# Optimization experiments

Hardware: AMD Instinct MI355X
Metric: run time of the kernel (lower is better)

## Reference

```python
import jax, jax.numpy as jnp
import numpy as np

H = 128           # hidden_size
N_NODE = 100000   # item vocab
B = 1024          # sessions
NODES_PER = 50
N = B * NODES_PER # total session nodes
E = 8 * N         # edges


def setup_inputs() -> dict:
    key = jax.random.key(0)
    ks = jax.random.split(key, 16)
    stdv = 1.0 / np.sqrt(H)
    u = lambda k, shape: jax.random.uniform(k, shape, jnp.float32, -stdv, stdv)
    x = jax.random.randint(ks[0], (N,), 1, N_NODE + 1)      # 1-indexed items
    edge_index = jax.random.randint(ks[1], (2, E), 0, N)
    batch = jnp.repeat(jnp.arange(B), NODES_PER)            # sorted segment ids
    return {
        "x": x, "edge_index": edge_index, "batch": batch,
        "emb_weight": u(ks[2], (N_NODE, H)),
        "W_gconv": u(ks[3], (H, H)),
        "W_ih": u(ks[4], (3 * H, H)), "W_hh": u(ks[5], (3 * H, H)),
        "b_ih": u(ks[6], (3 * H,)), "b_hh": u(ks[7], (3 * H,)),
        "W1_w": u(ks[8], (H, H)), "W1_b": u(ks[9], (H,)),
        "W2_w": u(ks[10], (H, H)), "W2_b": u(ks[11], (H,)),
        "q_w": u(ks[12], (1, H)), "q_b": u(ks[13], (1,)),
        "W3_w": u(ks[14], (H, 2 * H)), "W3_b": u(ks[15], (H,)),
    }


def _forward(x, edge_index, batch, emb_weight, W_gconv, W_ih, W_hh, b_ih, b_hh,
             W1_w, W1_b, W2_w, W2_b, q_w, q_b, W3_w, W3_b):
    n = x.shape[0]
    h = emb_weight[x - 1]                                   # [N, H]
    # GatedGraphConv, num_layers=1: linear -> scatter-add -> GRUCell
    m = h @ W_gconv                                          # [N, H]
    agg = jax.ops.segment_sum(m[edge_index[0]], edge_index[1], num_segments=n)
    gi = agg @ W_ih.T + b_ih                                 # [N, 3H]
    gh = h @ W_hh.T + b_hh
    i_r, i_z, i_n = jnp.split(gi, 3, axis=1)
    h_r, h_z, h_n = jnp.split(gh, 3, axis=1)
    r = jax.nn.sigmoid(i_r + h_r)
    z = jax.nn.sigmoid(i_z + h_z)
    ng = jnp.tanh(i_n + r * h_n)
    h = (1.0 - z) * ng + z * h
    h = jax.nn.relu(h)
    # Embedding2Score: segment-wise attention readout
    last_idx = jax.ops.segment_max(jnp.arange(n), batch, num_segments=B)
    v_n = h[last_idx]                                        # [B, H] last node per session
    a = jax.nn.sigmoid(v_n[batch] @ W1_w.T + W1_b + h @ W2_w.T + W2_b)
    alpha = a @ q_w.T + q_b                                  # [N, 1]
    s_g = jax.ops.segment_sum(alpha * h, batch, num_segments=B)  # [B, H]
    s_h = jnp.concatenate([v_n, s_g], axis=1) @ W3_w.T + W3_b    # [B, H]
    return s_h @ emb_weight.T                                # [B, n_node]


def reference(x, edge_index, batch, emb_weight, W_gconv, W_ih, W_hh, b_ih, b_hh,
              W1_w, W1_b, W2_w, W2_b, q_w, q_b, W3_w, W3_b):
    return _forward(x, edge_index, batch, emb_weight, W_gconv, W_ih, W_hh, b_ih, b_hh,
                    W1_w, W1_b, W2_w, W2_b, q_w, q_b, W3_w, W3_b)
```

## Files before the change

### kernel.cpp

```cpp
#include <hip/hip_runtime.h>
#include <math.h>

#define NNODES 51200
#define NEDGES 409600
#define NB 1024
#define NODES_PER 50
#define NVOCAB 100000
#define NVPAD 100096
#define SLOTS 64

typedef __attribute__((ext_vector_type(8))) short bf16x8;
typedef __attribute__((ext_vector_type(4))) float f32x4;

__device__ __forceinline__ float sigf(float x) { return 1.0f / (1.0f + __expf(-x)); }

__device__ __forceinline__ ushort f2bf(float x) {
    union { float f; unsigned u; } v; v.f = x;
    const unsigned r = v.u + 0x7FFF + ((v.u >> 16) & 1);
    return (ushort)(r >> 16);
}
__device__ __forceinline__ float bf2f(ushort u) {
    union { float f; unsigned u; } v; v.u = ((unsigned)u) << 16; return v.f;
}
__device__ __forceinline__ bf16x8 cvt8(const float* __restrict__ src) {
    const float4 v0 = *(const float4*)src, v1 = *(const float4*)(src + 4);
    bf16x8 p;
    p[0] = (short)f2bf(v0.x); p[1] = (short)f2bf(v0.y);
    p[2] = (short)f2bf(v0.z); p[3] = (short)f2bf(v0.w);
    p[4] = (short)f2bf(v1.x); p[5] = (short)f2bf(v1.y);
    p[6] = (short)f2bf(v1.z); p[7] = (short)f2bf(v1.w);
    return p;
}

__global__ __launch_bounds__(256)
void prep_kernel(const int* __restrict__ x, const float* __restrict__ emb,
                 ushort* __restrict__ hb, const int* __restrict__ ei,
                 int* __restrict__ cnt, int* __restrict__ esrc,
                 ushort* __restrict__ embswz, const float* __restrict__ Wih,
                 const float* __restrict__ Wg, ushort* __restrict__ Wc) {
    const int bid = blockIdx.x;
    const int t = threadIdx.x;
    if (bid < 3200) {
        const int tid = bid * 256 + t;
        const int i = tid >> 4, c8 = (tid & 15) * 8;
        const int idx = x[i] - 1;
        *(bf16x8*)(hb + (size_t)i * 128 + c8) = cvt8(emb + (size_t)idx * 128 + c8);
    } else if (bid < 4800) {
        const int e = (bid - 3200) * 256 + t;
        const int dst = ei[NEDGES + e];
        const int pos = atomicAdd(&cnt[dst], 1);
        if (pos < SLOTS) esrc[(size_t)dst * SLOTS + pos] = ei[e];
    } else if (bid < 11056) {
        const int f = (bid - 4800) * 256 + t;
        const int row = f >> 4, c8 = (f & 15) * 8;
        bf16x8 pk = {0, 0, 0, 0, 0, 0, 0, 0};
        if (row < NVOCAB) pk = cvt8(emb + (size_t)row * 128 + c8);
        *(bf16x8*)&embswz[(size_t)row * 128 + (c8 ^ ((row & 7) << 3))] = pk;
    } else {
        const int idx = (bid - 11056) * 256 + t;
        const int mrow = idx >> 7, n = idx & 127;
        const float* wr = Wih + (size_t)mrow * 128;
        const float* gr = Wg + (size_t)n * 128;
        float acc = 0.f;
        #pragma unroll 8
        for (int k = 0; k < 128; ++k)
            acc = fmaf(wr[k], gr[k], acc);
        Wc[idx] = f2bf(acc);
    }
}

__global__ __launch_bounds__(256)
void agg_kernel(const int* __restrict__ cnt, const int* __restrict__ esrc,
                const ushort* __restrict__ hb, ushort* __restrict__ aggb) {
    const int node = blockIdx.x * 4 + (threadIdx.x >> 6);
    const int l = threadIdx.x & 63;
    int cn = cnt[node]; if (cn > SLOTS) cn = SLOTS;
    const int* es = esrc + (size_t)node * SLOTS;
    float ax = 0.f, ay = 0.f;
    for (int j = 0; j < cn; ++j) {
        const int src = es[j];
        const unsigned u = *(const unsigned*)(hb + (size_t)src * 128 + l * 2);
        ax += bf2f((ushort)(u & 0xffff));
        ay += bf2f((ushort)(u >> 16));
    }
    const unsigned o = (unsigned)f2bf(ax) | ((unsigned)f2bf(ay) << 16);
    *(unsigned*)(aggb + (size_t)node * 128 + l * 2) = o;
}

__global__ __launch_bounds__(512)
void gru_fused(const ushort* __restrict__ aggb, const ushort* __restrict__ Wc,
               const float* __restrict__ Whh, const float* __restrict__ bih,
               const float* __restrict__ bhh, ushort* __restrict__ hb) {
    __shared__ ushort As[128 * 128];
    __shared__ ushort Bs[384 * 128];
    const int m0 = blockIdx.x * 128;
    const int t = threadIdx.x;
    const int lane = t & 63, wid = t >> 6;
    const int l15 = lane & 15, kg = (lane >> 4) * 8;

    #pragma unroll
    for (int f = t; f < 2048; f += 512) {
        const int r = f >> 4, c8 = (f & 15) * 8;
        const bf16x8 pk = *(const bf16x8*)(aggb + (size_t)(m0 + r) * 128 + c8);
        *(bf16x8*)&As[r * 128 + (c8 ^ ((r & 7) << 3))] = pk;
    }
    #pragma unroll
    for (int f = t; f < 6144; f += 512) {
        const int r = f >> 4, c8 = (f & 15) * 8;
        const bf16x8 pk = *(const bf16x8*)(Wc + (size_t)r * 128 + c8);
        *(bf16x8*)&Bs[r * 128 + (c8 ^ ((r & 7) << 3))] = pk;
    }
    __syncthreads();

    f32x4 gi[24] = {};
    #pragma unroll
    for (int kc = 0; kc < 4; ++kc) {
        const int cs = kc * 32 + kg;
        const int ra = wid * 16 + l15;
        const bf16x8 af = *(const bf16x8*)&As[ra * 128 + (cs ^ ((ra & 7) << 3))];
        #pragma unroll
        for (int j = 0; j < 24; ++j) {
            const int rb = j * 16 + l15;
            const bf16x8 bfr = *(const bf16x8*)&Bs[rb * 128 + (cs ^ ((rb & 7) << 3))];
            gi[j] = __builtin_amdgcn_mfma_f32_16x16x32_bf16(af, bfr, gi[j], 0, 0, 0);
        }
    }
    __syncthreads();

    #pragma unroll
    for (int f = t; f < 2048; f += 512) {
        const int r = f >> 4, c8 = (f & 15) * 8;
        const bf16x8 pk = *(const bf16x8*)(hb + (size_t)(m0 + r) * 128 + c8);
        *(bf16x8*)&As[r * 128 + (c8 ^ ((r & 7) << 3))] = pk;
    }
    #pragma unroll
    for (int f = t; f < 6144; f += 512) {
        const int r = f >> 4, c8 = (f & 15) * 8;
        *(bf16x8*)&Bs[r * 128 + (c8 ^ ((r & 7) << 3))] = cvt8(Whh + (size_t)r * 128 + c8);
    }
    __syncthreads();

    f32x4 gh[24] = {};
    #pragma unroll
    for (int kc = 0; kc < 4; ++kc) {
        const int cs = kc * 32 + kg;
        const int ra = wid * 16 + l15;
        const bf16x8 af = *(const bf16x8*)&As[ra * 128 + (cs ^ ((ra & 7) << 3))];
        #pragma unroll
        for (int j = 0; j < 24; ++j) {
            const int rb = j * 16 + l15;
            const bf16x8 bfr = *(const bf16x8*)&Bs[rb * 128 + (cs ^ ((rb & 7) << 3))];
            gh[j] = __builtin_amdgcn_mfma_f32_16x16x32_bf16(af, bfr, gh[j], 0, 0, 0);
        }
    }

    const int lr0 = wid * 16 + (lane >> 4) * 4;
    #pragma unroll
    for (int j = 0; j < 8; ++j) {
        const int col = j * 16 + l15;
        const float bir = bih[col], biz = bih[128 + col], bin = bih[256 + col];
        const float bhr = bhh[col], bhz = bhh[128 + col], bhn = bhh[256 + col];
        #pragma unroll
        for (int q = 0; q < 4; ++q) {
            const int lr = lr0 + q;
            const int adr = lr * 128 + (col ^ ((lr & 7) << 3));
            const float hv = bf2f(As[adr]);
            const float r_ = sigf(gi[j][q] + bir + gh[j][q] + bhr);
            const float z  = sigf(gi[j + 8][q] + biz + gh[j + 8][q] + bhz);
            const float ng = tanhf(gi[j + 16][q] + bin + r_ * (gh[j + 16][q] + bhn));
            As[adr] = f2bf(fmaxf((1.f - z) * ng + z * hv, 0.f));
        }
    }
    __syncthreads();
    #pragma unroll
    for (int f = t; f < 2048; f += 512) {
        const int r = f >> 4, c8 = (f & 15) * 8;
        *(bf16x8*)(hb + (size_t)(m0 + r) * 128 + c8) =
            *(const bf16x8*)&As[r * 128 + (c8 ^ ((r & 7) << 3))];
    }
}

__global__ __launch_bounds__(256)
void attn_sh(const ushort* __restrict__ hb, const float* __restrict__ W1,
             const float* __restrict__ b1, const float* __restrict__ W2,
             const float* __restrict__ qw, const float* __restrict__ qbp,
             const float* __restrict__ b2, const float* __restrict__ W3,
             const float* __restrict__ b3, ushort* __restrict__ shb) {
    __shared__ ushort As[128 * 128];
    __shared__ ushort Bs[128 * 128];
    __shared__ float t1s[2][128];
    __shared__ float qws[128];
    __shared__ float apar[2][2][64];
    __shared__ float alph[2][64];
    __shared__ float sgs[2][128];
    const int m0 = blockIdx.x * 100;
    const int t = threadIdx.x;
    const int lane = t & 63, wid = t >> 6;
    const int wr = wid >> 1, wc = wid & 1;
    const int l15 = lane & 15, kg = (lane >> 4) * 8;
    const int cr0 = (lane >> 4) * 4;

    #pragma unroll
    for (int f = t; f < 2048; f += 256) {
        const int r = f >> 4, c8 = (f & 15) * 8;
        int gr = m0 + r; if (gr > NNODES - 1) gr = NNODES - 1;
        *(bf16x8*)&As[r * 128 + (c8 ^ ((r & 7) << 3))] =
            *(const bf16x8*)(hb + (size_t)gr * 128 + c8);
        *(bf16x8*)&Bs[r * 128 + (c8 ^ ((r & 7) << 3))] = cvt8(W2 + (size_t)r * 128 + c8);
    }
    if (t < 128) qws[t] = qw[t];
    __syncthreads();

    f32x4 acc[4][4] = {};
    #pragma unroll
    for (int kc = 0; kc < 4; ++kc) {
        const int cs = kc * 32 + kg;
        bf16x8 af[4], bfr[4];
        #pragma unroll
        for (int i = 0; i < 4; ++i) {
            const int ra = wr * 64 + i * 16 + l15;
            af[i] = *(const bf16x8*)&As[ra * 128 + (cs ^ ((ra & 7) << 3))];
            const int rb = wc * 64 + i * 16 + l15;
            bfr[i] = *(const bf16x8*)&Bs[rb * 128 + (cs ^ ((rb & 7) << 3))];
        }
        #pragma unroll
        for (int i = 0; i < 4; ++i)
            #pragma unroll
            for (int j = 0; j < 4; ++j)
                acc[i][j] = __builtin_amdgcn_mfma_f32_16x16x32_bf16(af[i], bfr[j], acc[i][j], 0, 0, 0);
    }
    __syncthreads();

    #pragma unroll
    for (int j = 0; j < 4; ++j) {
        const int col = wc * 64 + j * 16 + l15;
        const int csw = (col & 7) << 3;
        #pragma unroll
        for (int i = 0; i < 4; ++i) {
            const int row = wr * 64 + i * 16 + cr0;
            #pragma unroll
            for (int q = 0; q < 4; ++q)
                Bs[col * 128 + ((row + q) ^ csw)] = f2bf(acc[i][j][q]);
        }
    }

    const int sess = wid >> 1, half = wid & 1;
    const int d = half * 64 + lane;
    const int vrow = sess * 50 + 49;
    const int vsw = (vrow & 7) << 3;
    float t1v = b1[d] + b2[d];
    const float* w1r = W1 + (size_t)d * 128;
    #pragma unroll 8
    for (int k = 0; k < 128; k += 4) {
        const float4 w = *(const float4*)(w1r + k);
        t1v += w.x * bf2f(As[vrow * 128 + ((k + 0) ^ vsw)])
             + w.y * bf2f(As[vrow * 128 + ((k + 1) ^ vsw)])
             + w.z * bf2f(As[vrow * 128 + ((k + 2) ^ vsw)])
             + w.w * bf2f(As[vrow * 128 + ((k + 3) ^ vsw)]);
    }
    t1s[sess][d] = t1v;
    __syncthreads();

    float p = 0.f;
    if (lane < 50) {
        const int row = sess * 50 + lane;
        const int d0 = half * 64;
        #pragma unroll 8
        for (int dd = d0; dd < d0 + 64; ++dd)
            p += qws[dd] * sigf(t1s[sess][dd] + bf2f(Bs[dd * 128 + (row ^ ((dd & 7) << 3))]));
    }
    apar[sess][half][lane] = p;
    __syncthreads();
    if (half == 0 && lane < 50)
        alph[sess][lane] = apar[sess][0][lane] + apar[sess][1][lane] + qbp[0];
    __syncthreads();

    float sacc = 0.f;
    #pragma unroll 10
    for (int i = 0; i < 50; ++i) {
        const int row = sess * 50 + i;
        sacc += alph[sess][i] * bf2f(As[row * 128 + (d ^ ((row & 7) << 3))]);
    }
    sgs[sess][d] = sacc;
    __syncthreads();

    float shacc = b3[d];
    const float* w3r = W3 + (size_t)d * 256;
    #pragma unroll 8
    for (int k = 0; k < 128; k += 4) {
        const float4 w = *(const float4*)(w3r + k);
        shacc += w.x * bf2f(As[vrow * 128 + ((k + 0) ^ vsw)])
               + w.y * bf2f(As[vrow * 128 + ((k + 1) ^ vsw)])
               + w.z * bf2f(As[vrow * 128 + ((k + 2) ^ vsw)])
               + w.w * bf2f(As[vrow * 128 + ((k + 3) ^ vsw)]);
    }
    #pragma unroll 8
    for (int k = 0; k < 128; k += 4) {
        const float4 w = *(const float4*)(w3r + 128 + k);
        shacc += w.x * sgs[sess][k] + w.y * sgs[sess][k + 1]
               + w.z * sgs[sess][k + 2] + w.w * sgs[sess][k + 3];
    }
    const int orow = blockIdx.x * 2 + sess;
    shb[(size_t)orow * 128 + (d ^ ((orow & 7) << 3))] = f2bf(shacc);
}

__global__ __launch_bounds__(256)
void gemm_vocab(float* __restrict__ C, const ushort* __restrict__ Ab,
                const ushort* __restrict__ Bswz) {
    __shared__ ushort As[128 * 128];
    __shared__ ushort Bs[128 * 128];
    float* Cs = (float*)Bs;
    const int id = blockIdx.x;
    const int xcd = id & 7, loc = id >> 3;
    const int mt = loc & 7, gin = loc >> 3;
    const int grp = xcd * 25 + gin;
    const int m0 = mt * 128;
    const int t = threadIdx.x;
    const int lane = t & 63, wid = t >> 6;
    const int wr = wid >> 1, wc = wid & 1;
    const int l15 = lane & 15, kg = (lane >> 4) * 8;
    const int cr0 = (lane >> 4) * 4;

    #pragma unroll
    for (int f = t; f < 2048; f += 256)
        *(bf16x8*)&As[f * 8] = *(const bf16x8*)(Ab + (size_t)m0 * 128 + f * 8);

    for (int it = 0; it < 4; ++it) {
        const int n0 = (grp * 4 + it) * 128;
        if (n0 >= NVOCAB) break;
        __syncthreads();
        const ushort* srcb = Bswz + (size_t)n0 * 128;
        #pragma unroll
        for (int f = t; f < 2048; f += 256)
            *(bf16x8*)&Bs[f * 8] = *(const bf16x8*)(srcb + f * 8);
        __syncthreads();

        f32x4 acc[4][4] = {};
        #pragma unroll
        for (int kc = 0; kc < 4; ++kc) {
            const int cs = kc * 32 + kg;
            bf16x8 af[4], bfr[4];
            #pragma unroll
            for (int i = 0; i < 4; ++i) {
                const int ra = wr * 64 + i * 16 + l15;
                af[i] = *(const bf16x8*)&As[ra * 128 + (cs ^ ((ra & 7) << 3))];
                const int rb = wc * 64 + i * 16 + l15;
                bfr[i] = *(const bf16x8*)&Bs[rb * 128 + (cs ^ ((rb & 7) << 3))];
            }
            #pragma unroll
            for (int i = 0; i < 4; ++i)
                #pragma unroll
                for (int j = 0; j < 4; ++j)
                    acc[i][j] = __builtin_amdgcn_mfma_f32_16x16x32_bf16(af[i], bfr[j], acc[i][j], 0, 0, 0);
        }
        __syncthreads();

        #pragma unroll
        for (int half = 0; half < 2; ++half) {
            if (wr == half) {
                #pragma unroll
                for (int j = 0; j < 4; ++j) {
                    const int col = wc * 64 + j * 16 + l15;
                    #pragma unroll
                    for (int i = 0; i < 4; ++i) {
                        const int rl = i * 16 + cr0;
                        #pragma unroll
                        for (int q = 0; q < 4; ++q)
                            Cs[(rl + q) * 128 + col] = acc[i][j][q];
                    }
                }
            }
            __syncthreads();
            #pragma unroll
            for (int f = t; f < 2048; f += 256) {
                const int r = f >> 5, c4 = (f & 31) * 4;
                if (n0 + c4 < NVOCAB) {
                    const f32x4 v = *(const f32x4*)&Cs[r * 128 + c4];
                    *(f32x4*)(C + (size_t)(m0 + half * 64 + r) * NVOCAB + n0 + c4) = v;
                }
            }
            __syncthreads();
        }
    }
}

extern "C" void kernel_launch(void* const* d_in, const int* in_sizes, int n_in,
                              void* d_out, int out_size, void* d_ws, size_t ws_size,
                              hipStream_t stream) {
    const int*   x   = (const int*)d_in[0];
    const int*   ei  = (const int*)d_in[1];
    const float* emb = (const float*)d_in[3];
    const float* Wg  = (const float*)d_in[4];
    const float* Wih = (const float*)d_in[5];
    const float* Whh = (const float*)d_in[6];
    const float* bih = (const float*)d_in[7];
    const float* bhh = (const float*)d_in[8];
    const float* W1  = (const float*)d_in[9];
    const float* b1  = (const float*)d_in[10];
    const float* W2  = (const float*)d_in[11];
    const float* b2  = (const float*)d_in[12];
    const float* qw  = (const float*)d_in[13];
    const float* qb  = (const float*)d_in[14];
    const float* W3  = (const float*)d_in[15];
    const float* b3  = (const float*)d_in[16];
    float* out = (float*)d_out;

    float*  ws     = (float*)d_ws;
    ushort* hb     = (ushort*)ws;
    ushort* aggb   = (ushort*)(ws + 3276800);
    ushort* Wc     = (ushort*)(ws + 6553600);
    ushort* shb    = (ushort*)(ws + 6578176);
    ushort* embswz = (ushort*)(ws + 6643712);
    int*    cnt    = (int*)(ws + 13049856);
    int*    esrc   = cnt + NNODES;

    hipMemsetAsync(cnt, 0, NNODES * sizeof(int), stream);

    prep_kernel<<<11248, 256, 0, stream>>>(x, emb, hb, ei, cnt, esrc, embswz,
                                           Wih, Wg, Wc);

    agg_kernel<<<12800, 256, 0, stream>>>(cnt, esrc, hb, aggb);

    gru_fused<<<400, 512, 0, stream>>>(aggb, Wc, Whh, bih, bhh, hb);

    attn_sh<<<512, 256, 0, stream>>>(hb, W1, b1, W2, qw, qb, b2, W3, b3, shb);

    gemm_vocab<<<1600, 256, 0, stream>>>(out, shb, embswz);
}
```

Before: 322.0 us.

## Fuse edge aggregation into GRU kernel, pre-convert weights, and widen vocab GEMM grid

Measured after the change: 413.3 us. +28.3%, slower.

```diff
diff --git a/kernel.cpp b/kernel.cpp
--- a/kernel.cpp
+++ b/kernel.cpp
@@ -37,7 +37,9 @@
                  ushort* __restrict__ hb, const int* __restrict__ ei,
                  int* __restrict__ cnt, int* __restrict__ esrc,
                  ushort* __restrict__ embswz, const float* __restrict__ Wih,
-                 const float* __restrict__ Wg, ushort* __restrict__ Wc) {
+                 const float* __restrict__ Wg, ushort* __restrict__ Wc,
+                 const float* __restrict__ Whh, ushort* __restrict__ Whhb,
+                 const float* __restrict__ W2, ushort* __restrict__ W2b) {
     const int bid = blockIdx.x;
     const int t = threadIdx.x;
     if (bid < 3200) {
@@ -56,7 +58,7 @@
         bf16x8 pk = {0, 0, 0, 0, 0, 0, 0, 0};
         if (row < NVOCAB) pk = cvt8(emb + (size_t)row * 128 + c8);
         *(bf16x8*)&embswz[(size_t)row * 128 + (c8 ^ ((row & 7) << 3))] = pk;
-    } else {
+    } else if (bid < 11248) {
         const int idx = (bid - 11056) * 256 + t;
         const int mrow = idx >> 7, n = idx & 127;
         const float* wr = Wih + (size_t)mrow * 128;
@@ -65,32 +67,23 @@
         #pragma unroll 8
         for (int k = 0; k < 128; ++k)
             acc = fmaf(wr[k], gr[k], acc);
-        Wc[idx] = f2bf(acc);
-    }
-}
-
-__global__ __launch_bounds__(256)
-void agg_kernel(const int* __restrict__ cnt, const int* __restrict__ esrc,
-                const ushort* __restrict__ hb, ushort* __restrict__ aggb) {
-    const int node = blockIdx.x * 4 + (threadIdx.x >> 6);
-    const int l = threadIdx.x & 63;
-    int cn = cnt[node]; if (cn > SLOTS) cn = SLOTS;
-    const int* es = esrc + (size_t)node * SLOTS;
-    float ax = 0.f, ay = 0.f;
-    for (int j = 0; j < cn; ++j) {
-        const int src = es[j];
-        const unsigned u = *(const unsigned*)(hb + (size_t)src * 128 + l * 2);
-        ax += bf2f((ushort)(u & 0xffff));
-        ay += bf2f((ushort)(u >> 16));
-    }
-    const unsigned o = (unsigned)f2bf(ax) | ((unsigned)f2bf(ay) << 16);
-    *(unsigned*)(aggb + (size_t)node * 128 + l * 2) = o;
+        Wc[mrow * 128 + (n ^ ((mrow & 7) << 3))] = f2bf(acc);
+    } else if (bid < 11272) {
+        const int f = (bid - 11248) * 256 + t;
+        const int r = f >> 4, c8 = (f & 15) * 8;
+        *(bf16x8*)&Whhb[r * 128 + (c8 ^ ((r & 7) << 3))] = cvt8(Whh + (size_t)r * 128 + c8);
+    } else {
+        const int f = (bid - 11272) * 256 + t;
+        const int r = f >> 4, c8 = (f & 15) * 8;
+        *(bf16x8*)&W2b[r * 128 + (c8 ^ ((r & 7) << 3))] = cvt8(W2 + (size_t)r * 128 + c8);
+    }
 }
 
 __global__ __launch_bounds__(512)
-void gru_fused(const ushort* __restrict__ aggb, const ushort* __restrict__ Wc,
-               const float* __restrict__ Whh, const float* __restrict__ bih,
-               const float* __restrict__ bhh, ushort* __restrict__ hb) {
+void gru_fused(const int* __restrict__ cnt, const int* __restrict__ esrc,
+               const ushort* __restrict__ hb, const ushort* __restrict__ Wc,
+               const ushort* __restrict__ Whhb, const float* __restrict__ bih,
+               const float* __restrict__ bhh, ushort* __restrict__ hnew) {
     __shared__ ushort As[128 * 128];
     __shared__ ushort Bs[384 * 128];
     const int m0 = blockIdx.x * 128;
@@ -99,17 +92,24 @@
     const int l15 = lane & 15, kg = (lane >> 4) * 8;
 
     #pragma unroll
-    for (int f = t; f < 2048; f += 512) {
-        const int r = f >> 4, c8 = (f & 15) * 8;
-        const bf16x8 pk = *(const bf16x8*)(aggb + (size_t)(m0 + r) * 128 + c8);
-        *(bf16x8*)&As[r * 128 + (c8 ^ ((r & 7) << 3))] = pk;
-    }
-    #pragma unroll
-    for (int f = t; f < 6144; f += 512) {
-        const int r = f >> 4, c8 = (f & 15) * 8;
-        const bf16x8 pk = *(const bf16x8*)(Wc + (size_t)r * 128 + c8);
-        *(bf16x8*)&Bs[r * 128 + (c8 ^ ((r & 7) << 3))] = pk;
-    }
+    for (int rr = 0; rr < 16; ++rr) {
+        const int r = wid * 16 + rr;
+        const int node = m0 + r;
+        int cn = cnt[node]; if (cn > SLOTS) cn = SLOTS;
+        const int* es = esrc + (size_t)node * SLOTS;
+        float ax = 0.f, ay = 0.f;
+        for (int j = 0; j < cn; ++j) {
+            const int src = es[j];
+            const unsigned u = *(const unsigned*)(hb + (size_t)src * 128 + lane * 2);
+            ax += bf2f((ushort)(u & 0xffff));
+            ay += bf2f((ushort)(u >> 16));
+        }
+        const unsigned o = (unsigned)f2bf(ax) | ((unsigned)f2bf(ay) << 16);
+        *(unsigned*)&As[r * 128 + ((lane * 2) ^ ((r & 7) << 3))] = o;
+    }
+    #pragma unroll
+    for (int f = t; f < 6144; f += 512)
+        *(bf16x8*)&Bs[f * 8] = *(const bf16x8*)(Wc + (size_t)f * 8);
     __syncthreads();
 
     f32x4 gi[24] = {};
@@ -134,10 +134,8 @@
         *(bf16x8*)&As[r * 128 + (c8 ^ ((r & 7) << 3))] = pk;
     }
     #pragma unroll
-    for (int f = t; f < 6144; f += 512) {
-        const int r = f >> 4, c8 = (f & 15) * 8;
-        *(bf16x8*)&Bs[r * 128 + (c8 ^ ((r & 7) << 3))] = cvt8(Whh + (size_t)r * 128 + c8);
-    }
+    for (int f = t; f < 6144; f += 512)
+        *(bf16x8*)&Bs[f * 8] = *(const bf16x8*)(Whhb + (size_t)f * 8);
     __syncthreads();
 
     f32x4 gh[24] = {};
@@ -175,14 +173,14 @@
     #pragma unroll
     for (int f = t; f < 2048; f += 512) {
         const int r = f >> 4, c8 = (f & 15) * 8;
-        *(bf16x8*)(hb + (size_t)(m0 + r) * 128 + c8) =
+        *(bf16x8*)(hnew + (size_t)(m0 + r) * 128 + c8) =
             *(const bf16x8*)&As[r * 128 + (c8 ^ ((r & 7) << 3))];
     }
 }
 
 __global__ __launch_bounds__(256)
 void attn_sh(const ushort* __restrict__ hb, const float* __restrict__ W1,
-             const float* __restrict__ b1, const float* __restrict__ W2,
+             const float* __restrict__ b1, const ushort* __restrict__ W2b,
              const float* __restrict__ qw, const float* __restrict__ qbp,
              const float* __restrict__ b2, const float* __restrict__ W3,
              const float* __restrict__ b3, ushort* __restrict__ shb) {
@@ -206,7 +204,7 @@
         int gr = m0 + r; if (gr > NNODES - 1) gr = NNODES - 1;
         *(bf16x8*)&As[r * 128 + (c8 ^ ((r & 7) << 3))] =
             *(const bf16x8*)(hb + (size_t)gr * 128 + c8);
-        *(bf16x8*)&Bs[r * 128 + (c8 ^ ((r & 7) << 3))] = cvt8(W2 + (size_t)r * 128 + c8);
+        *(bf16x8*)&Bs[f * 8] = *(const bf16x8*)(W2b + (size_t)f * 8);
     }
     if (t < 128) qws[t] = qw[t];
     __syncthreads();
@@ -312,8 +310,9 @@
     float* Cs = (float*)Bs;
     const int id = blockIdx.x;
     const int xcd = id & 7, loc = id >> 3;
-    const int mt = loc & 7, gin = loc >> 3;
-    const int grp = xcd * 25 + gin;
+    const int mt = loc & 7, g = loc >> 3;
+    const int grp = xcd * 49 + g;
+    if (grp * 256 >= NVOCAB) return;
     const int m0 = mt * 128;
     const int t = threadIdx.x;
     const int lane = t & 63, wid = t >> 6;
@@ -325,8 +324,8 @@
     for (int f = t; f < 2048; f += 256)
         *(bf16x8*)&As[f * 8] = *(const bf16x8*)(Ab + (size_t)m0 * 128 + f * 8);
 
-    for (int it = 0; it < 4; ++it) {
-        const int n0 = (grp * 4 + it) * 128;
+    for (int it = 0; it < 2; ++it) {
+        const int n0 = (grp * 2 + it) * 128;
         if (n0 >= NVOCAB) break;
         __syncthreads();
         const ushort* srcb = Bswz + (size_t)n0 * 128;
@@ -407,23 +406,23 @@
 
     float*  ws     = (float*)d_ws;
     ushort* hb     = (ushort*)ws;
-    ushort* aggb   = (ushort*)(ws + 3276800);
+    ushort* hnew   = (ushort*)(ws + 3276800);
     ushort* Wc     = (ushort*)(ws + 6553600);
-    ushort* shb    = (ushort*)(ws + 6578176);
-    ushort* embswz = (ushort*)(ws + 6643712);
-    int*    cnt    = (int*)(ws + 13049856);
+    ushort* Whhb   = (ushort*)(ws + 6578176);
+    ushort* W2b    = (ushort*)(ws + 6602752);
+    ushort* shb    = (ushort*)(ws + 6610944);
+    ushort* embswz = (ushort*)(ws + 6676480);
+    int*    cnt    = (int*)(ws + 13082624);
     int*    esrc   = cnt + NNODES;
 
     hipMemsetAsync(cnt, 0, NNODES * sizeof(int), stream);
 
-    prep_kernel<<<11248, 256, 0, stream>>>(x, emb, hb, ei, cnt, esrc, embswz,
-                                           Wih, Wg, Wc);
-
-    agg_kernel<<<12800, 256, 0, stream>>>(cnt, esrc, hb, aggb);
-
-    gru_fused<<<400, 512, 0, stream>>>(aggb, Wc, Whh, bih, bhh, hb);
-
-    attn_sh<<<512, 256, 0, stream>>>(hb, W1, b1, W2, qw, qb, b2, W3, b3, shb);
-
-    gemm_vocab<<<1600, 256, 0, stream>>>(out, shb, embswz);
-}
+    prep_kernel<<<11280, 256, 0, stream>>>(x, emb, hb, ei, cnt, esrc, embswz,
+                                           Wih, Wg, Wc, Whh, Whhb, W2, W2b);
+
+    gru_fused<<<400, 512, 0, stream>>>(cnt, esrc, hb, Wc, Whhb, bih, bhh, hnew);
+
+    attn_sh<<<512, 256, 0, stream>>>(hnew, W1, b1, W2b, qw, qb, b2, W3, b3, shb);
+
+    gemm_vocab<<<3136, 256, 0, stream>>>(out, shb, embswz);
+}
```
